# Optimization experiments

Hardware: AMD Instinct MI355X
Metric: run time of the kernel (lower is better)

## Reference

```python
import jax, jax.numpy as jnp
import numpy as np

N_EMBD = 1024
N_HEAD = 16
B, T, T_MEM = 4, 1024, 1024


def setup_inputs() -> dict:
    key = jax.random.key(0)
    ks = jax.random.split(key, 11)
    s = 1.0 / np.sqrt(N_EMBD)
    return {
        "q_in": jax.random.normal(ks[0], (B, T, N_EMBD), jnp.float32),
        "k_in": jax.random.normal(ks[1], (B, T_MEM, N_EMBD), jnp.float32),
        "v_in": jax.random.normal(ks[2], (B, T_MEM, N_EMBD), jnp.float32),
        # torch nn.Linear weights: [out_features, in_features]
        "Wq": jax.random.normal(ks[3], (N_EMBD, N_EMBD), jnp.float32) * s,
        "bq": jax.random.normal(ks[4], (N_EMBD,), jnp.float32) * s,
        "Wk": jax.random.normal(ks[5], (N_EMBD, N_EMBD), jnp.float32) * s,
        "bk": jax.random.normal(ks[6], (N_EMBD,), jnp.float32) * s,
        "Wv": jax.random.normal(ks[7], (N_EMBD, N_EMBD), jnp.float32) * s,
        "bv": jax.random.normal(ks[8], (N_EMBD,), jnp.float32) * s,
        "Wo": jax.random.normal(ks[9], (N_EMBD, N_EMBD), jnp.float32) * s,
        "bo": jax.random.normal(ks[10], (N_EMBD,), jnp.float32) * s,
    }


def reference(q_in, k_in, v_in, Wq, bq, Wk, bk, Wv, bv, Wo, bo):
    b, t, c = q_in.shape
    t_mem = k_in.shape[1]
    hd = c // N_HEAD  # head dim

    def proj(x, W, bias):
        return x @ W.T + bias

    # [b, h, t, hd]
    q = proj(q_in, Wq, bq).reshape(b, t, N_HEAD, hd).transpose(0, 2, 1, 3)
    k = proj(k_in, Wk, bk).reshape(b, t_mem, N_HEAD, hd).transpose(0, 2, 1, 3)
    v = proj(v_in, Wv, bv).reshape(b, t_mem, N_HEAD, hd).transpose(0, 2, 1, 3)

    scale = 1.0 / np.sqrt(hd).astype(np.float32)
    att = jnp.einsum("bhqd,bhkd->bhqk", q, k) * scale
    att = jax.nn.softmax(att, axis=-1)  # dropout p=0 -> identity

    y = jnp.einsum("bhqk,bhkd->bhqd", att, v)
    y = y.transpose(0, 2, 1, 3).reshape(b, t, c)
    y = proj(y, Wo, bo)  # resid_drop p=0 -> identity

    attention = jnp.mean(att, axis=1)  # mean over heads: [b, t, t_mem]
    return (y, attention)
```

## Files before the change

kernel.cpp:

```cpp
#include <hip/hip_runtime.h>
#include <hip/hip_fp16.h>


typedef __attribute__((ext_vector_type(8))) short s16x8;
typedef __attribute__((ext_vector_type(4))) float f32x4;
typedef __attribute__((ext_vector_type(4))) unsigned short u16x4;

#define N_EMBD 1024
#define NH 16
#define BT 4096
#define STR 1032
#define SM_SHIFT 16.0f

#if __has_builtin(__builtin_amdgcn_global_load_lds)
#define HAVE_GLL 1
#define GLDS16(g, l)                                                              \
  __builtin_amdgcn_global_load_lds((__attribute__((address_space(1))) void*)(g), \
                                   (__attribute__((address_space(3))) void*)(l), 16, 0, 0)
#else
#define HAVE_GLL 0
#endif

static __device__ __forceinline__ unsigned short f2bf(float f) {
  unsigned int u = __builtin_bit_cast(unsigned int, f);
  u += 0x7FFFu + ((u >> 16) & 1u);
  return (unsigned short)(u >> 16);
}
static __device__ __forceinline__ float bf2f(unsigned short h) {
  return __builtin_bit_cast(float, ((unsigned int)h) << 16);
}
static __device__ __forceinline__ unsigned int pk_bf16(float lo, float hi) {
  unsigned int r;
  asm("v_cvt_pk_bf16_f32 %0, %1, %2" : "=v"(r) : "v"(lo), "v"(hi));
  return r;
}

__global__ __launch_bounds__(256) void cvt_in3(const float* __restrict__ q,
                                               const float* __restrict__ k,
                                               const float* __restrict__ v,
                                               unsigned short* __restrict__ out) {
  const int z = blockIdx.z;
  const float* src = (z == 0) ? q : (z == 1 ? k : v);
  int i = (blockIdx.x * 256 + threadIdx.x) * 4;
  float4 val = *(const float4*)(src + i);
  u16x4 o;
  o[0] = f2bf(val.x);
  o[1] = f2bf(val.y);
  o[2] = f2bf(val.z);
  o[3] = f2bf(val.w);
  *(u16x4*)(out + (size_t)z * BT * N_EMBD + i) = o;
}

__global__ __launch_bounds__(256) void cvt_w4(const float* __restrict__ wo,
                                              const float* __restrict__ wq,
                                              const float* __restrict__ wk,
                                              const float* __restrict__ wv,
                                              unsigned short* __restrict__ out) {
  const int z = blockIdx.z;
  const float* src = (z == 0) ? wo : (z == 1 ? wq : (z == 2 ? wk : wv));
  const float scale = (z == 1) ? 0.125f : 1.0f;
  int i = (blockIdx.x * 256 + threadIdx.x) * 4;
  float4 val = *(const float4*)(src + i);
  u16x4 o;
  o[0] = f2bf(val.x * scale);
  o[1] = f2bf(val.y * scale);
  o[2] = f2bf(val.z * scale);
  o[3] = f2bf(val.w * scale);
  *(u16x4*)(out + (size_t)z * N_EMBD * N_EMBD + i) = o;
}

template <bool F32OUT>
static __device__ __forceinline__ void gemm_bt_tile(const unsigned short* __restrict__ A,
                                                    const unsigned short* __restrict__ B,
                                                    const float* __restrict__ bias, float bscale,
                                                    void* __restrict__ Cout,
                                                    int m0, int n0, int N, int K,
                                                    unsigned short* Al, unsigned short* Bl) {
  const int tid = threadIdx.x;
  const int l = tid & 63, w = tid >> 6;
  const int wr = w >> 1, wc = w & 1;
  const int l15 = l & 15, l4 = l >> 4;
  const int srow = tid >> 3;
  const int skk = (tid & 7) * 8;
  f32x4 acc[4][4] = {};
  for (int k0 = 0; k0 < K; k0 += 64) {
#if HAVE_GLL
#pragma unroll
    for (int i = 0; i < 4; ++i) {
      GLDS16(&A[(size_t)(m0 + i * 32 + srow) * K + k0 + skk], Al + i * 2048 + w * 512);
      GLDS16(&B[(size_t)(n0 + i * 32 + srow) * K + k0 + skk], Bl + i * 2048 + w * 512);
    }
#else
#pragma unroll
    for (int i = 0; i < 4; ++i) {
      int row = i * 32 + srow;
      *(s16x8*)&Al[row * 64 + skk] = *(const s16x8*)&A[(size_t)(m0 + row) * K + k0 + skk];
      *(s16x8*)&Bl[row * 64 + skk] = *(const s16x8*)&B[(size_t)(n0 + row) * K + k0 + skk];
    }
#endif
    __syncthreads();
#pragma unroll
    for (int kf = 0; kf < 2; ++kf) {
      s16x8 af[4], bfr[4];
#pragma unroll
      for (int mi = 0; mi < 4; ++mi)
        af[mi] = *(const s16x8*)&Al[(wr * 64 + mi * 16 + l15) * 64 + kf * 32 + l4 * 8];
#pragma unroll
      for (int nj = 0; nj < 4; ++nj)
        bfr[nj] = *(const s16x8*)&Bl[(wc * 64 + nj * 16 + l15) * 64 + kf * 32 + l4 * 8];
#pragma unroll
      for (int mi = 0; mi < 4; ++mi) {
#pragma unroll
        for (int nj = 0; nj < 4; ++nj)
          acc[mi][nj] =
              __builtin_amdgcn_mfma_f32_16x16x32_bf16(af[mi], bfr[nj], acc[mi][nj], 0, 0, 0);
      }
    }
    __syncthreads();
  }
#pragma unroll
  for (int nj = 0; nj < 4; ++nj) {
    int col = n0 + wc * 64 + nj * 16 + l15;
    float bv = bias[col] * bscale;
#pragma unroll
    for (int mi = 0; mi < 4; ++mi) {
#pragma unroll
      for (int r = 0; r < 4; ++r) {
        int row = m0 + wr * 64 + mi * 16 + l4 * 4 + r;
        float v = acc[mi][nj][r] + bv;
        if constexpr (F32OUT)
          ((float*)Cout)[(size_t)row * N + col] = v;
        else
          ((unsigned short*)Cout)[(size_t)row * N + col] = f2bf(v);
      }
    }
  }
}

__global__ __launch_bounds__(256) void gemm_qkv(const unsigned short* __restrict__ Xin,
                                                const unsigned short* __restrict__ Wbf,
                                                const float* __restrict__ bq,
                                                const float* __restrict__ bk,
                                                const float* __restrict__ bv,
                                                unsigned short* __restrict__ Cout) {
  __shared__ unsigned short Al[128 * 64];
  __shared__ unsigned short Bl[128 * 64];
  const int z = blockIdx.z;
  const float* bias = (z == 0) ? bq : (z == 1 ? bk : bv);
  const float bscale = (z == 0) ? 0.125f : 1.0f;
  gemm_bt_tile<false>(Xin + (size_t)z * BT * N_EMBD,
                      Wbf + (size_t)(1 + z) * N_EMBD * N_EMBD, bias, bscale,
                      Cout + (size_t)z * BT * N_EMBD, blockIdx.x * 128, blockIdx.y * 128,
                      N_EMBD, N_EMBD, Al, Bl);
}

__global__ __launch_bounds__(256) void gemm_out(const unsigned short* __restrict__ Ybf,
                                                const unsigned short* __restrict__ Wo,
                                                const float* __restrict__ bo,
                                                float* __restrict__ Cout) {
  __shared__ unsigned short Al[128 * 64];
  __shared__ unsigned short Bl[128 * 64];
  gemm_bt_tile<true>(Ybf, Wo, bo, 1.0f, Cout, blockIdx.x * 128, blockIdx.y * 128, N_EMBD, N_EMBD,
                     Al, Bl);
}

__global__ __launch_bounds__(256) void transpose_v(const unsigned short* __restrict__ Vp,
                                                   unsigned short* __restrict__ Vt) {
  __shared__ unsigned short tile[64][65];
  const int t0 = blockIdx.x * 64, h = blockIdx.y, b = blockIdx.z;
  const int r = threadIdx.x >> 2, c0 = (threadIdx.x & 3) * 16;
  const unsigned short* src = Vp + (size_t)(b * 1024 + t0 + r) * 1024 + h * 64 + c0;
#pragma unroll
  for (int j = 0; j < 16; ++j) tile[r][c0 + j] = src[j];
  __syncthreads();
  unsigned short* dst = Vt + (size_t)((b * 16 + h) * 64 + r) * 1024 + t0 + c0;
#pragma unroll
  for (int j = 0; j < 16; ++j) dst[j] = tile[c0 + j][r];
}

__global__ __launch_bounds__(1024, 4) void attn_ph2(const unsigned short* __restrict__ Qp,
                                                    const unsigned short* __restrict__ Kp,
                                                    const unsigned short* __restrict__ Vt,
                                                    unsigned short* __restrict__ Ybf,
                                                    unsigned short* __restrict__ Pmean) {
  __shared__ __align__(16) unsigned short S2[2][32 * STR];
  __shared__ float RedS[2][32][8];
  const int tid = threadIdx.x;
  const int tm = tid >> 9;
  const int ttid = tid & 511;
  const int w4 = ttid >> 6;
  const int l = tid & 63;
  const int l15 = l & 15, l4 = l >> 4;
  const int qgw = w4 >> 2;
  const int dtw = w4 & 3;

  const int bid = blockIdx.x;
  const int grp = bid & 7, qt = bid >> 3;
  const int b = grp >> 1, hg = grp & 1;
  const int q0 = qt * 32;

  __half2 am[32];
#pragma unroll
  for (int j = 0; j < 32; ++j) am[j] = __float2half2_rn(0.f);

#pragma unroll 1
  for (int it = 0; it < 4; ++it) {
    const int h = hg * 8 + it * 2 + tm;
    const unsigned short* qb0 = Qp + (size_t)(b * 1024 + q0 + l15) * 1024 + h * 64 + l4 * 8;
    const unsigned short* qb1 = qb0 + (size_t)16 * 1024;
    s16x8 aq00 = *(const s16x8*)qb0;
    s16x8 aq01 = *(const s16x8*)(qb0 + 32);
    s16x8 aq10 = *(const s16x8*)qb1;
    s16x8 aq11 = *(const s16x8*)(qb1 + 32);
    float ps0 = 0.f, ps1 = 0.f;
    __builtin_amdgcn_s_setprio(1);
#pragma unroll
    for (int nt = 0; nt < 8; ++nt) {
      int gn = w4 * 8 + nt;
      const unsigned short* kb = Kp + (size_t)(b * 1024 + gn * 16 + l15) * 1024 + h * 64 + l4 * 8;
      s16x8 kf0 = *(const s16x8*)kb;
      s16x8 kf1 = *(const s16x8*)(kb + 32);
      f32x4 s0 = {}, s1 = {};
      s0 = __builtin_amdgcn_mfma_f32_16x16x32_bf16(kf0, aq00, s0, 0, 0, 0);
      s0 = __builtin_amdgcn_mfma_f32_16x16x32_bf16(kf1, aq01, s0, 0, 0, 0);
      s1 = __builtin_amdgcn_mfma_f32_16x16x32_bf16(kf0, aq10, s1, 0, 0, 0);
      s1 = __builtin_amdgcn_mfma_f32_16x16x32_bf16(kf1, aq11, s1, 0, 0, 0);
      float e00 = __expf(s0[0] - SM_SHIFT);
      float e01 = __expf(s0[1] - SM_SHIFT);
      float e02 = __expf(s0[2] - SM_SHIFT);
      float e03 = __expf(s0[3] - SM_SHIFT);
      float e10 = __expf(s1[0] - SM_SHIFT);
      float e11 = __expf(s1[1] - SM_SHIFT);
      float e12 = __expf(s1[2] - SM_SHIFT);
      float e13 = __expf(s1[3] - SM_SHIFT);
      ps0 += (e00 + e01) + (e02 + e03);
      ps1 += (e10 + e11) + (e12 + e13);
      uint2 p0, p1;
      p0.x = pk_bf16(e00, e01);
      p0.y = pk_bf16(e02, e03);
      p1.x = pk_bf16(e10, e11);
      p1.y = pk_bf16(e12, e13);
      *(uint2*)&S2[tm][l15 * STR + gn * 16 + l4 * 4] = p0;
      *(uint2*)&S2[tm][(16 + l15) * STR + gn * 16 + l4 * 4] = p1;
    }
    __builtin_amdgcn_s_setprio(0);
    ps0 += __shfl_xor(ps0, 16);
    ps0 += __shfl_xor(ps0, 32);
    ps1 += __shfl_xor(ps1, 16);
    ps1 += __shfl_xor(ps1, 32);
    if (l < 16) {
      RedS[tm][l][w4] = ps0;
      RedS[tm][16 + l][w4] = ps1;
    }
    __syncthreads();

    float lsA = 0.f;
#pragma unroll
    for (int j = 0; j < 8; ++j) lsA += RedS[tm][qgw * 16 + l15][j];
    float fac = 0.0625f / lsA;
    f32x4 y = {};
    const unsigned short* vb =
        Vt + (size_t)((b * 16 + h) * 64 + dtw * 16 + l15) * 1024 + l4 * 8;
    __builtin_amdgcn_s_setprio(1);
#pragma unroll
    for (int kq = 0; kq < 4; ++kq) {
#pragma unroll
      for (int kk = 0; kk < 8; ++kk) {
        const int ks = kq * 8 + kk;
        s16x8 pa = *(const s16x8*)&S2[tm][(qgw * 16 + l15) * STR + ks * 32 + l4 * 8];
        y = __builtin_amdgcn_mfma_f32_16x16x32_bf16(pa, *(const s16x8*)(vb + ks * 32), y, 0, 0, 0);
        if (kq == dtw) {
#pragma unroll
          for (int e2 = 0; e2 < 4; ++e2) {
            float2 fv;
            fv.x = bf2f((unsigned short)pa[e2 * 2]) * fac;
            fv.y = bf2f((unsigned short)pa[e2 * 2 + 1]) * fac;
            am[kk * 4 + e2] = __hadd2(am[kk * 4 + e2], __float22half2_rn(fv));
          }
        }
      }
    }
    __builtin_amdgcn_s_setprio(0);
#pragma unroll
    for (int rr = 0; rr < 4; ++rr) {
      int row = qgw * 16 + l4 * 4 + rr;
      float lsr = 0.f;
#pragma unroll
      for (int j = 0; j < 8; ++j) lsr += RedS[tm][row][j];
      Ybf[(size_t)(b * 1024 + q0 + row) * 1024 + h * 64 + dtw * 16 + l15] = f2bf(y[rr] / lsr);
    }
    __syncthreads();
  }

  unsigned int* us = (unsigned int*)S2;
  if (tm == 1) {
#pragma unroll
    for (int j = 0; j < 32; ++j) us[ttid * 32 + j] = __builtin_bit_cast(unsigned int, am[j]);
  }
  __syncthreads();
  if (tm == 0) {
    unsigned short* pm = Pmean + ((size_t)(b * 2 + hg) << 20) +
                         (size_t)(q0 + qgw * 16 + l15) * 1024 + dtw * 256 + l4 * 8;
#pragma unroll
    for (int kk = 0; kk < 8; ++kk) {
      s16x8 ov;
#pragma unroll
      for (int e2 = 0; e2 < 4; ++e2) {
        int j = kk * 4 + e2;
        __half2 ot = __builtin_bit_cast(__half2, us[ttid * 32 + j]);
        float2 fo = __half22float2(ot);
        float2 fm = __half22float2(am[j]);
        ov[e2 * 2] = (short)f2bf(fm.x + fo.x);
        ov[e2 * 2 + 1] = (short)f2bf(fm.y + fo.y);
      }
      *(s16x8*)&pm[kk * 32] = ov;
    }
  }
}

__global__ __launch_bounds__(256) void mean2(const unsigned short* __restrict__ P2,
                                             float* __restrict__ out) {
  size_t f = ((size_t)blockIdx.x * 256 + threadIdx.x) * 8;
  int b = (int)(f >> 20);
  size_t i0 = f + ((size_t)b << 20);
  s16x8 a = *(const s16x8*)&P2[i0];
  s16x8 d = *(const s16x8*)&P2[i0 + (1u << 20)];
  float4 o0, o1;
  o0.x = bf2f((unsigned short)a[0]) + bf2f((unsigned short)d[0]);
  o0.y = bf2f((unsigned short)a[1]) + bf2f((unsigned short)d[1]);
  o0.z = bf2f((unsigned short)a[2]) + bf2f((unsigned short)d[2]);
  o0.w = bf2f((unsigned short)a[3]) + bf2f((unsigned short)d[3]);
  o1.x = bf2f((unsigned short)a[4]) + bf2f((unsigned short)d[4]);
  o1.y = bf2f((unsigned short)a[5]) + bf2f((unsigned short)d[5]);
  o1.z = bf2f((unsigned short)a[6]) + bf2f((unsigned short)d[6]);
  o1.w = bf2f((unsigned short)a[7]) + bf2f((unsigned short)d[7]);
  *(float4*)&out[f] = o0;
  *(float4*)&out[f + 4] = o1;
}

extern "C" void kernel_launch(void* const* d_in, const int* in_sizes, int n_in, void* d_out,
                              int out_size, void* d_ws, size_t ws_size, hipStream_t stream) {
  const float* q_in = (const float*)d_in[0];
  const float* k_in = (const float*)d_in[1];
  const float* v_in = (const float*)d_in[2];
  const float* Wq = (const float*)d_in[3];
  const float* bq = (const float*)d_in[4];
  const float* Wk = (const float*)d_in[5];
  const float* bk = (const float*)d_in[6];
  const float* Wv = (const float*)d_in[7];
  const float* bv = (const float*)d_in[8];
  const float* Wo = (const float*)d_in[9];
  const float* bo = (const float*)d_in[10];

  float* out_y = (float*)d_out;
  float* out_att = out_y + (size_t)BT * N_EMBD;

  char* ws = (char*)d_ws;
  const size_t MB = 1024 * 1024;
  unsigned short* xin_bf = (unsigned short*)(ws);
  unsigned short* W_bf = (unsigned short*)(ws + 24 * MB);
  unsigned short* Qp = (unsigned short*)(ws + 32 * MB);
  unsigned short* Kp = Qp + (size_t)BT * N_EMBD;
  unsigned short* Vp = Kp + (size_t)BT * N_EMBD;
  unsigned short* Pmean = (unsigned short*)(ws);
  unsigned short* Vt = (unsigned short*)(ws + 16 * MB);
  unsigned short* Ybf = Vp;

  const int NIN = BT * N_EMBD;
  const int NW = N_EMBD * N_EMBD;

  cvt_in3<<<dim3(NIN / 1024, 1, 3), 256, 0, stream>>>(q_in, k_in, v_in, xin_bf);
  cvt_w4<<<dim3(NW / 1024, 1, 4), 256, 0, stream>>>(Wo, Wq, Wk, Wv, W_bf);

  gemm_qkv<<<dim3(BT / 128, N_EMBD / 128, 3), 256, 0, stream>>>(xin_bf, W_bf, bq, bk, bv, Qp);
  transpose_v<<<dim3(16, 16, 4), 256, 0, stream>>>(Vp, Vt);
  attn_ph2<<<256, 1024, 0, stream>>>(Qp, Kp, Vt, Ybf, Pmean);
  mean2<<<2048, 256, 0, stream>>>(Pmean, out_att);
  gemm_out<<<dim3(BT / 128, N_EMBD / 128), 256, 0, stream>>>(Ybf, W_bf, bo, out_y);
}
```

Baseline: 208.2 us.

## Split attention block into producer/consumer warp groups pipelined across heads

The attention kernel previously had two 512-thread halves, each running QK^T/exp and then PV for its own head, with two heads per iteration. Now waves 0-7 compute the scores and exponentials for head it into a double-buffered LDS slot while waves 8-15 run the PV matmul and the head-mean accumulation for head it-1. This overlaps the exp-heavy score phase with the MFMA-heavy PV phase. It also removes the final LDS merge of the two halves' mean accumulators. The cost is nine barriered stages instead of four, and each wave group idles during one pipeline fill or drain stage.

```diff
diff --git a/kernel.cpp b/kernel.cpp
--- a/kernel.cpp
+++ b/kernel.cpp
@@ -178,21 +178,20 @@
   for (int j = 0; j < 16; ++j) dst[j] = tile[c0 + j][r];
 }
 
-__global__ __launch_bounds__(1024, 4) void attn_ph2(const unsigned short* __restrict__ Qp,
-                                                    const unsigned short* __restrict__ Kp,
-                                                    const unsigned short* __restrict__ Vt,
-                                                    unsigned short* __restrict__ Ybf,
-                                                    unsigned short* __restrict__ Pmean) {
+__global__ __launch_bounds__(1024, 4) void attn_pc(const unsigned short* __restrict__ Qp,
+                                                   const unsigned short* __restrict__ Kp,
+                                                   const unsigned short* __restrict__ Vt,
+                                                   unsigned short* __restrict__ Ybf,
+                                                   unsigned short* __restrict__ Pmean) {
   __shared__ __align__(16) unsigned short S2[2][32 * STR];
   __shared__ float RedS[2][32][8];
   const int tid = threadIdx.x;
-  const int tm = tid >> 9;
-  const int ttid = tid & 511;
-  const int w4 = ttid >> 6;
+  const int w = tid >> 6;
   const int l = tid & 63;
   const int l15 = l & 15, l4 = l >> 4;
-  const int qgw = w4 >> 2;
-  const int dtw = w4 & 3;
+  const int cw = w & 7;
+  const int qgw = cw >> 2;
+  const int dtw = cw & 3;
 
   const int bid = blockIdx.x;
   const int grp = bid & 7, qt = bid >> 3;
@@ -204,101 +203,99 @@
   for (int j = 0; j < 32; ++j) am[j] = __float2half2_rn(0.f);
 
 #pragma unroll 1
-  for (int it = 0; it < 4; ++it) {
-    const int h = hg * 8 + it * 2 + tm;
-    const unsigned short* qb0 = Qp + (size_t)(b * 1024 + q0 + l15) * 1024 + h * 64 + l4 * 8;
-    const unsigned short* qb1 = qb0 + (size_t)16 * 1024;
-    s16x8 aq00 = *(const s16x8*)qb0;
-    s16x8 aq01 = *(const s16x8*)(qb0 + 32);
-    s16x8 aq10 = *(const s16x8*)qb1;
-    s16x8 aq11 = *(const s16x8*)(qb1 + 32);
-    float ps0 = 0.f, ps1 = 0.f;
-    __builtin_amdgcn_s_setprio(1);
-#pragma unroll
-    for (int nt = 0; nt < 8; ++nt) {
-      int gn = w4 * 8 + nt;
-      const unsigned short* kb = Kp + (size_t)(b * 1024 + gn * 16 + l15) * 1024 + h * 64 + l4 * 8;
-      s16x8 kf0 = *(const s16x8*)kb;
-      s16x8 kf1 = *(const s16x8*)(kb + 32);
-      f32x4 s0 = {}, s1 = {};
-      s0 = __builtin_amdgcn_mfma_f32_16x16x32_bf16(kf0, aq00, s0, 0, 0, 0);
-      s0 = __builtin_amdgcn_mfma_f32_16x16x32_bf16(kf1, aq01, s0, 0, 0, 0);
-      s1 = __builtin_amdgcn_mfma_f32_16x16x32_bf16(kf0, aq10, s1, 0, 0, 0);
-      s1 = __builtin_amdgcn_mfma_f32_16x16x32_bf16(kf1, aq11, s1, 0, 0, 0);
-      float e00 = __expf(s0[0] - SM_SHIFT);
-      float e01 = __expf(s0[1] - SM_SHIFT);
-      float e02 = __expf(s0[2] - SM_SHIFT);
-      float e03 = __expf(s0[3] - SM_SHIFT);
-      float e10 = __expf(s1[0] - SM_SHIFT);
-      float e11 = __expf(s1[1] - SM_SHIFT);
-      float e12 = __expf(s1[2] - SM_SHIFT);
-      float e13 = __expf(s1[3] - SM_SHIFT);
-      ps0 += (e00 + e01) + (e02 + e03);
-      ps1 += (e10 + e11) + (e12 + e13);
-      uint2 p0, p1;
-      p0.x = pk_bf16(e00, e01);
-      p0.y = pk_bf16(e02, e03);
-      p1.x = pk_bf16(e10, e11);
-      p1.y = pk_bf16(e12, e13);
-      *(uint2*)&S2[tm][l15 * STR + gn * 16 + l4 * 4] = p0;
-      *(uint2*)&S2[tm][(16 + l15) * STR + gn * 16 + l4 * 4] = p1;
-    }
-    __builtin_amdgcn_s_setprio(0);
-    ps0 += __shfl_xor(ps0, 16);
-    ps0 += __shfl_xor(ps0, 32);
-    ps1 += __shfl_xor(ps1, 16);
-    ps1 += __shfl_xor(ps1, 32);
-    if (l < 16) {
-      RedS[tm][l][w4] = ps0;
-      RedS[tm][16 + l][w4] = ps1;
-    }
-    __syncthreads();
-
-    float lsA = 0.f;
-#pragma unroll
-    for (int j = 0; j < 8; ++j) lsA += RedS[tm][qgw * 16 + l15][j];
-    float fac = 0.0625f / lsA;
-    f32x4 y = {};
-    const unsigned short* vb =
-        Vt + (size_t)((b * 16 + h) * 64 + dtw * 16 + l15) * 1024 + l4 * 8;
-    __builtin_amdgcn_s_setprio(1);
-#pragma unroll
-    for (int kq = 0; kq < 4; ++kq) {
-#pragma unroll
-      for (int kk = 0; kk < 8; ++kk) {
-        const int ks = kq * 8 + kk;
-        s16x8 pa = *(const s16x8*)&S2[tm][(qgw * 16 + l15) * STR + ks * 32 + l4 * 8];
-        y = __builtin_amdgcn_mfma_f32_16x16x32_bf16(pa, *(const s16x8*)(vb + ks * 32), y, 0, 0, 0);
-        if (kq == dtw) {
-#pragma unroll
-          for (int e2 = 0; e2 < 4; ++e2) {
-            float2 fv;
-            fv.x = bf2f((unsigned short)pa[e2 * 2]) * fac;
-            fv.y = bf2f((unsigned short)pa[e2 * 2 + 1]) * fac;
-            am[kk * 4 + e2] = __hadd2(am[kk * 4 + e2], __float22half2_rn(fv));
+  for (int it = 0; it <= 8; ++it) {
+    if (w < 8 && it < 8) {
+      const int h = hg * 8 + it;
+      const int bufi = it & 1;
+      const unsigned short* qb0 = Qp + (size_t)(b * 1024 + q0 + l15) * 1024 + h * 64 + l4 * 8;
+      const unsigned short* qb1 = qb0 + (size_t)16 * 1024;
+      s16x8 aq00 = *(const s16x8*)qb0;
+      s16x8 aq01 = *(const s16x8*)(qb0 + 32);
+      s16x8 aq10 = *(const s16x8*)qb1;
+      s16x8 aq11 = *(const s16x8*)(qb1 + 32);
+      float ps0 = 0.f, ps1 = 0.f;
+#pragma unroll
+      for (int nt = 0; nt < 8; ++nt) {
+        int gn = w * 8 + nt;
+        const unsigned short* kb =
+            Kp + (size_t)(b * 1024 + gn * 16 + l15) * 1024 + h * 64 + l4 * 8;
+        s16x8 kf0 = *(const s16x8*)kb;
+        s16x8 kf1 = *(const s16x8*)(kb + 32);
+        f32x4 s0 = {}, s1 = {};
+        s0 = __builtin_amdgcn_mfma_f32_16x16x32_bf16(kf0, aq00, s0, 0, 0, 0);
+        s0 = __builtin_amdgcn_mfma_f32_16x16x32_bf16(kf1, aq01, s0, 0, 0, 0);
+        s1 = __builtin_amdgcn_mfma_f32_16x16x32_bf16(kf0, aq10, s1, 0, 0, 0);
+        s1 = __builtin_amdgcn_mfma_f32_16x16x32_bf16(kf1, aq11, s1, 0, 0, 0);
+        float e00 = __expf(s0[0] - SM_SHIFT);
+        float e01 = __expf(s0[1] - SM_SHIFT);
+        float e02 = __expf(s0[2] - SM_SHIFT);
+        float e03 = __expf(s0[3] - SM_SHIFT);
+        float e10 = __expf(s1[0] - SM_SHIFT);
+        float e11 = __expf(s1[1] - SM_SHIFT);
+        float e12 = __expf(s1[2] - SM_SHIFT);
+        float e13 = __expf(s1[3] - SM_SHIFT);
+        ps0 += (e00 + e01) + (e02 + e03);
+        ps1 += (e10 + e11) + (e12 + e13);
+        uint2 p0, p1;
+        p0.x = pk_bf16(e00, e01);
+        p0.y = pk_bf16(e02, e03);
+        p1.x = pk_bf16(e10, e11);
+        p1.y = pk_bf16(e12, e13);
+        *(uint2*)&S2[bufi][l15 * STR + gn * 16 + l4 * 4] = p0;
+        *(uint2*)&S2[bufi][(16 + l15) * STR + gn * 16 + l4 * 4] = p1;
+      }
+      ps0 += __shfl_xor(ps0, 16);
+      ps0 += __shfl_xor(ps0, 32);
+      ps1 += __shfl_xor(ps1, 16);
+      ps1 += __shfl_xor(ps1, 32);
+      if (l < 16) {
+        RedS[bufi][l][w] = ps0;
+        RedS[bufi][16 + l][w] = ps1;
+      }
+    } else if (w >= 8 && it > 0) {
+      const int h = hg * 8 + (it - 1);
+      const int bufi = (it - 1) & 1;
+      float lsA = 0.f;
+#pragma unroll
+      for (int j = 0; j < 8; ++j) lsA += RedS[bufi][qgw * 16 + l15][j];
+      float fac = 0.0625f / lsA;
+      f32x4 y = {};
+      const unsigned short* vb =
+          Vt + (size_t)((b * 16 + h) * 64 + dtw * 16 + l15) * 1024 + l4 * 8;
+      __builtin_amdgcn_s_setprio(1);
+#pragma unroll
+      for (int kq = 0; kq < 4; ++kq) {
+#pragma unroll
+        for (int kk = 0; kk < 8; ++kk) {
+          const int ks = kq * 8 + kk;
+          s16x8 pa = *(const s16x8*)&S2[bufi][(qgw * 16 + l15) * STR + ks * 32 + l4 * 8];
+          y = __builtin_amdgcn_mfma_f32_16x16x32_bf16(pa, *(const s16x8*)(vb + ks * 32), y, 0,
+                                                      0, 0);
+          if (kq == dtw) {
+#pragma unroll
+            for (int e2 = 0; e2 < 4; ++e2) {
+              float2 fv;
+              fv.x = bf2f((unsigned short)pa[e2 * 2]) * fac;
+              fv.y = bf2f((unsigned short)pa[e2 * 2 + 1]) * fac;
+              am[kk * 4 + e2] = __hadd2(am[kk * 4 + e2], __float22half2_rn(fv));
+            }
           }
         }
       }
-    }
-    __builtin_amdgcn_s_setprio(0);
-#pragma unroll
-    for (int rr = 0; rr < 4; ++rr) {
-      int row = qgw * 16 + l4 * 4 + rr;
-      float lsr = 0.f;
-#pragma unroll
-      for (int j = 0; j < 8; ++j) lsr += RedS[tm][row][j];
-      Ybf[(size_t)(b * 1024 + q0 + row) * 1024 + h * 64 + dtw * 16 + l15] = f2bf(y[rr] / lsr);
+      __builtin_amdgcn_s_setprio(0);
+#pragma unroll
+      for (int rr = 0; rr < 4; ++rr) {
+        int row = qgw * 16 + l4 * 4 + rr;
+        float lsr = 0.f;
+#pragma unroll
+        for (int j = 0; j < 8; ++j) lsr += RedS[bufi][row][j];
+        Ybf[(size_t)(b * 1024 + q0 + row) * 1024 + h * 64 + dtw * 16 + l15] = f2bf(y[rr] / lsr);
+      }
     }
     __syncthreads();
   }
 
-  unsigned int* us = (unsigned int*)S2;
-  if (tm == 1) {
-#pragma unroll
-    for (int j = 0; j < 32; ++j) us[ttid * 32 + j] = __builtin_bit_cast(unsigned int, am[j]);
-  }
-  __syncthreads();
-  if (tm == 0) {
+  if (w >= 8) {
     unsigned short* pm = Pmean + ((size_t)(b * 2 + hg) << 20) +
                          (size_t)(q0 + qgw * 16 + l15) * 1024 + dtw * 256 + l4 * 8;
 #pragma unroll
@@ -306,12 +303,9 @@
       s16x8 ov;
 #pragma unroll
       for (int e2 = 0; e2 < 4; ++e2) {
-        int j = kk * 4 + e2;
-        __half2 ot = __builtin_bit_cast(__half2, us[ttid * 32 + j]);
-        float2 fo = __half22float2(ot);
-        float2 fm = __half22float2(am[j]);
-        ov[e2 * 2] = (short)f2bf(fm.x + fo.x);
-        ov[e2 * 2 + 1] = (short)f2bf(fm.y + fo.y);
+        float2 fm = __half22float2(am[kk * 4 + e2]);
+        ov[e2 * 2] = (short)f2bf(fm.x);
+        ov[e2 * 2 + 1] = (short)f2bf(fm.y);
       }
       *(s16x8*)&pm[kk * 32] = ov;
     }
@@ -374,7 +368,7 @@
 
   gemm_qkv<<<dim3(BT / 128, N_EMBD / 128, 3), 256, 0, stream>>>(xin_bf, W_bf, bq, bk, bv, Qp);
   transpose_v<<<dim3(16, 16, 4), 256, 0, stream>>>(Vp, Vt);
-  attn_ph2<<<256, 1024, 0, stream>>>(Qp, Kp, Vt, Ybf, Pmean);
+  attn_pc<<<256, 1024, 0, stream>>>(Qp, Kp, Vt, Ybf, Pmean);
   mean2<<<2048, 256, 0, stream>>>(Pmean, out_att);
   gemm_out<<<dim3(BT / 128, N_EMBD / 128), 256, 0, stream>>>(Ybf, W_bf, bo, out_y);
 }
```

Result: slower. 216.7 us (+4.1%).
